# Performance work log

Measured on AMD Instinct MI355X. Metric: run time of the kernel, lower is better.

The kernel has to match this reference:

```python
import jax, jax.numpy as jnp
import numpy as np

HEADS = 8
DIM_HEAD = 64
DIM = 512
B, N = 4, 2048
SCALE = DIM_HEAD ** -0.5


def setup_inputs() -> dict:
    key = jax.random.key(0)
    k1, k2, k3, k4, k5, k6 = jax.random.split(key, 6)
    inner = HEADS * DIM_HEAD
    s = DIM ** -0.5
    return {
        "input_feature": jax.random.normal(k1, (B, N, DIM), dtype=jnp.float32),
        "mask": jax.random.randint(k2, (B, N), 0, 2, dtype=jnp.int32),
        "Wq": jax.random.normal(k3, (inner, DIM), dtype=jnp.float32) * s,
        "Wk": jax.random.normal(k4, (inner, DIM), dtype=jnp.float32) * s,
        "Wv": jax.random.normal(k5, (inner, DIM), dtype=jnp.float32) * s,
        "Wout": jax.random.normal(k6, (DIM, inner), dtype=jnp.float32) * s,
    }


def reference(input_feature, mask, Wq, Wk, Wv, Wout):
    # Conv1d with kernel_size=1, no bias == per-token linear: out = W @ x_channels
    q = jnp.einsum('bnc,dc->bnd', input_feature, Wq)  # [B, N, H*Dh]
    k = jnp.einsum('bnc,dc->bnd', input_feature, Wk)
    v = jnp.einsum('bnc,dc->bnd', input_feature, Wv)

    # '(n c)' channel layout is head-major -> reshape to [B, N, H, Dh], move head out front
    def split_heads(t):
        return t.reshape(B, N, HEADS, DIM_HEAD).transpose(2, 0, 1, 3)  # [H, B, N, Dh]

    q, k, v = split_heads(q), split_heads(k), split_heads(v)

    scores = jnp.einsum('hbtd,hbsd->hbts', q, k) * SCALE  # [H, B, N, N]
    # masked_fill(mask == 0, 1e-9): fill with small CONSTANT (not -inf), faithful to source
    m = (mask == 0)[None, :, None, :]  # [1, B, 1, N]
    scores = jnp.where(m, jnp.float32(1e-9), scores)
    att = jax.nn.softmax(scores, axis=-1)
    out = jnp.einsum('hbts,hbsd->hbtd', att, v)  # [H, B, N, Dh]

    # '(n b) tokens c -> b (n c) tokens' : head-major channel concat
    out = out.transpose(1, 2, 0, 3).reshape(B, N, HEADS * DIM_HEAD)  # [B, N, H*Dh]
    out = jnp.einsum('bnd,ed->bne', out, Wout)  # [B, N, DIM]
    return out
```

## Files before the change

kernel.cpp:

```cpp
#include <hip/hip_runtime.h>
#include <hip/hip_bf16.h>

typedef __attribute__((ext_vector_type(8))) short short8;
typedef __attribute__((ext_vector_type(4))) short short4_t;
typedef __attribute__((ext_vector_type(4))) float float4_;

#define LOG2E 1.4426950408889634f

__device__ __forceinline__ short f2bf(float f) {
    unsigned int u = __builtin_bit_cast(unsigned int, f);
    u = (u + 0x7FFFu + ((u >> 16) & 1u)) >> 16;
    return (short)u;
}

__device__ __forceinline__ unsigned pk2bf(float a, float b) {
    unsigned ua = __builtin_bit_cast(unsigned, a) + 0x8000u;
    unsigned ub = __builtin_bit_cast(unsigned, b) + 0x8000u;
    return __builtin_amdgcn_perm(ub, ua, 0x07060302);
}

__device__ __forceinline__ void pl32swap(unsigned &a, unsigned &b) {
    auto r = __builtin_amdgcn_permlane32_swap(a, b, false, false);
    a = r[0]; b = r[1];
}
__device__ __forceinline__ void pl16swap(unsigned &a, unsigned &b) {
    auto r = __builtin_amdgcn_permlane16_swap(a, b, false, false);
    a = r[0]; b = r[1];
}

union U4 { unsigned u[4]; short8 s; };

__device__ __forceinline__ void gload_lds16(const short* g, short* l) {
    __builtin_amdgcn_global_load_lds((const __attribute__((address_space(1))) void*)g,
                                     (__attribute__((address_space(3))) void*)l, 16, 0, 0);
}

__global__ __launch_bounds__(256) void cvt_kernel(
    const float* __restrict__ X, const float* __restrict__ Wq, const float* __restrict__ Wk,
    const float* __restrict__ Wv, const float* __restrict__ Wo,
    short* __restrict__ Xb, short* __restrict__ Wqkvb, short* __restrict__ Wob) {
    int i = blockIdx.x * 256 + threadIdx.x;
    const float* src; short* dst; float sc = 1.0f;
    if (i < 1048576) { src = X + (size_t)i * 4; dst = Xb + (size_t)i * 4; }
    else {
        int w = i - 1048576; int sec = w >> 16; int j = (w & 65535) * 4;
        if (sec == 0)      { src = Wq + j; dst = Wqkvb + j; sc = 0.125f * LOG2E; }
        else if (sec == 1) { src = Wk + j; dst = Wqkvb + 262144 + j; }
        else if (sec == 2) { src = Wv + j; dst = Wqkvb + 524288 + j; }
        else               { src = Wo + j; dst = Wob + j; }
    }
    float4 v = *(const float4*)src;
    short4_t o;
    o[0] = f2bf(v.x * sc); o[1] = f2bf(v.y * sc); o[2] = f2bf(v.z * sc); o[3] = f2bf(v.w * sc);
    *(short4_t*)dst = o;
}

__global__ __launch_bounds__(256) void gemm_qkv(const short* __restrict__ A, const short* __restrict__ B,
                                                const int* __restrict__ mask,
                                                short* __restrict__ Qb, short* __restrict__ Kb,
                                                short* __restrict__ Vtb) {
    __shared__ __align__(16) short smemAB[2 * 8192];
    __shared__ int maskL[128];
    short* At = smemAB;
    short* Bt = smemAB + 8192;
    constexpr int K = 512;
    int tid = threadIdx.x;
    int wid = tid >> 6, lane = tid & 63;
    int quad = lane >> 4, cc = lane & 15;
    int c7 = cc & 7;
    int wr = wid >> 1, wc = wid & 1;
    int m0 = blockIdx.y * 128, n0 = blockIdx.x * 128;
    if (tid < 128) maskL[tid] = mask[m0 + tid];

    const short* gA[4]; const short* gB[4]; int lofs[4];
#pragma unroll
    for (int p = 0; p < 4; ++p) {
        int slot = p * 256 + tid;
        int r = slot >> 3, c = slot & 7;
        int cs = (c ^ (r & 7)) * 8;
        gA[p] = A + (size_t)(m0 + r) * K + cs;
        gB[p] = B + (size_t)(n0 + r) * K + cs;
        lofs[p] = slot * 8;
    }
    short8 arg[4], brg[4];
#pragma unroll
    for (int p = 0; p < 4; ++p) { arg[p] = *(const short8*)gA[p]; brg[p] = *(const short8*)gB[p]; }

    float4_ acc[4][4] = {};

    for (int kk = 0; kk < K; kk += 64) {
        __syncthreads();
#pragma unroll
        for (int p = 0; p < 4; ++p) {
            *(short8*)(At + lofs[p]) = arg[p];
            *(short8*)(Bt + lofs[p]) = brg[p];
        }
        if (kk < K - 64) {
#pragma unroll
            for (int p = 0; p < 4; ++p) {
                arg[p] = *(const short8*)(gA[p] + kk + 64);
                brg[p] = *(const short8*)(gB[p] + kk + 64);
            }
        }
        __syncthreads();
#pragma unroll
        for (int kc = 0; kc < 2; ++kc) {
            short8 af[4], bf[4];
#pragma unroll
            for (int i = 0; i < 4; ++i)
                af[i] = *(const short8*)(At + (wr * 64 + i * 16 + cc) * 64 + (((kc * 4 + quad) ^ c7) * 8));
#pragma unroll
            for (int j = 0; j < 4; ++j)
                bf[j] = *(const short8*)(Bt + (wc * 64 + j * 16 + cc) * 64 + (((kc * 4 + quad) ^ c7) * 8));
#pragma unroll
            for (int i = 0; i < 4; ++i)
#pragma unroll
                for (int j = 0; j < 4; ++j)
                    acc[i][j] = __builtin_amdgcn_mfma_f32_16x16x32_bf16(af[i], bf[j], acc[i][j], 0, 0, 0);
        }
    }

    int which = n0 >> 9;
    int b = m0 >> 11;
    if (which == 2) {
        __syncthreads();
        short* T = smemAB;
#pragma unroll
        for (int i = 0; i < 4; ++i) {
#pragma unroll
            for (int j = 0; j < 4; ++j) {
                int d_l = wc * 64 + j * 16 + cc;
                int nnb = wr * 64 + i * 16 + quad * 4;
                int G = nnb >> 3, half = (nnb >> 2) & 1;
                int Gs = G ^ (d_l & 15);
                short4_t pv;
                pv[0] = f2bf(acc[i][j][0]); pv[1] = f2bf(acc[i][j][1]);
                pv[2] = f2bf(acc[i][j][2]); pv[3] = f2bf(acc[i][j][3]);
                *(short4_t*)(T + d_l * 128 + Gs * 8 + half * 4) = pv;
            }
        }
        __syncthreads();
#pragma unroll
        for (int p = 0; p < 8; ++p) {
            int slot = p * 256 + tid;
            int d = slot >> 4, G = slot & 15;
            short8 v = *(const short8*)(T + d * 128 + ((G ^ (d & 15)) * 8));
            *(short8*)(Vtb + ((size_t)(b * 512 + (n0 & 511) + d)) * 2048 + (m0 & 2047) + G * 8) = v;
        }
    } else {
        short* dst = which ? Kb : Qb;
#pragma unroll
        for (int i = 0; i < 4; ++i) {
#pragma unroll
            for (int j = 0; j < 4; ++j) {
#pragma unroll
                for (int r = 0; r < 4; ++r) {
                    int lm = wr * 64 + i * 16 + quad * 4 + r;
                    int nn = (m0 & 2047) + lm;
                    int hd = (n0 & 511) + wc * 64 + j * 16 + cc;
                    int h = hd >> 6, dh = hd & 63;
                    float v = acc[i][j][r];
                    if (which == 1 && maskL[lm] == 0) v = 0.0f;
                    dst[((((size_t)b * 8 + h) * 2048 + nn) * 64) + dh] = f2bf(v);
                }
            }
        }
    }
}

__global__ __launch_bounds__(256, 4) void attn_kernel(const short* __restrict__ Q, const short* __restrict__ Kg,
                                                      const short* __restrict__ Vt,
                                                      short* __restrict__ AO) {
    __shared__ __align__(16) short KbufL[2 * 4096];
    __shared__ __align__(16) short VbufL[2 * 4096];

    int tid = threadIdx.x;
    int w = tid >> 6, lane = tid & 63;
    int quad = lane >> 4, cc = lane & 15;
    int c7 = cc & 7;
    int bh = blockIdx.x, b = bh >> 3, h = bh & 7;
    int t0 = blockIdx.y * 64 + w * 16;
    size_t kbase = (size_t)bh * 2048 * 64;
    size_t vbase = (size_t)b * 512 * 2048 + (size_t)h * 64 * 2048;

    short8 qf[2];
#pragma unroll
    for (int kc = 0; kc < 2; ++kc)
        qf[kc] = *(const short8*)(Q + kbase + (size_t)(t0 + cc) * 64 + kc * 32 + quad * 8);

    int koff[4][2];
#pragma unroll
    for (int rb = 0; rb < 4; ++rb)
#pragma unroll
        for (int kc = 0; kc < 2; ++kc)
            koff[rb][kc] = (rb * 16 + cc) * 64 + (((kc * 4 + quad) ^ c7) * 8);

    int sA = tid >> 3, cA = tid & 7;
    const short* gK0 = Kg + kbase + (size_t)sA * 64 + ((cA ^ (sA & 7)) * 8);
    const short* gK1 = gK0 + 32 * 64;
    const short* gV0 = Vt + vbase + (size_t)sA * 2048 + ((cA ^ (sA & 7)) * 8);
    const short* gV1 = gV0 + 32 * 2048;
    int ld0 = tid * 8, ld1 = tid * 8 + 2048;

    short8 krg0 = *(const short8*)gK0, krg1 = *(const short8*)gK1;
    short8 vrg0 = *(const short8*)gV0, vrg1 = *(const short8*)gV1;
    gK0 += 4096; gK1 += 4096; gV0 += 64; gV1 += 64;
    *(short8*)(KbufL + ld0) = krg0; *(short8*)(KbufL + ld1) = krg1;
    *(short8*)(VbufL + ld0) = vrg0; *(short8*)(VbufL + ld1) = vrg1;
    krg0 = *(const short8*)gK0; krg1 = *(const short8*)gK1;
    vrg0 = *(const short8*)gV0; vrg1 = *(const short8*)gV1;
    gK0 += 4096; gK1 += 4096; gV0 += 64; gV1 += 64;

    float4_ o[4] = {};
    float lp = 0.f;

#pragma unroll 2
    for (int it = 0; it < 32; ++it) {
        __syncthreads();
        int cur = it & 1;
        const short* Kt  = KbufL + cur * 4096;
        const short* Vtt = VbufL + cur * 4096;
        if (it < 31) {
            short* Kn = KbufL + (cur ^ 1) * 4096;
            short* Vn = VbufL + (cur ^ 1) * 4096;
            *(short8*)(Kn + ld0) = krg0; *(short8*)(Kn + ld1) = krg1;
            *(short8*)(Vn + ld0) = vrg0; *(short8*)(Vn + ld1) = vrg1;
        }
        if (it < 30) {
            krg0 = *(const short8*)gK0; krg1 = *(const short8*)gK1;
            vrg0 = *(const short8*)gV0; vrg1 = *(const short8*)gV1;
            gK0 += 4096; gK1 += 4096; gV0 += 64; gV1 += 64;
        }

        float4_ acc[4];
        __builtin_amdgcn_s_setprio(1);
#pragma unroll
        for (int sb = 0; sb < 4; ++sb) {
            short8 kf0 = *(const short8*)(Kt + koff[sb][0]);
            short8 kf1 = *(const short8*)(Kt + koff[sb][1]);
            float4_ z = {0.f, 0.f, 0.f, 0.f};
            z = __builtin_amdgcn_mfma_f32_16x16x32_bf16(kf0, qf[0], z, 0, 0, 0);
            acc[sb] = __builtin_amdgcn_mfma_f32_16x16x32_bf16(kf1, qf[1], z, 0, 0, 0);
        }
        __builtin_amdgcn_s_setprio(0);

        unsigned Wp[4][2];
#pragma unroll
        for (int sb = 0; sb < 4; ++sb) {
            float x0 = __builtin_amdgcn_exp2f(acc[sb][0]);
            float x1 = __builtin_amdgcn_exp2f(acc[sb][1]);
            float x2 = __builtin_amdgcn_exp2f(acc[sb][2]);
            float x3 = __builtin_amdgcn_exp2f(acc[sb][3]);
            lp += (x0 + x1) + (x2 + x3);
            Wp[sb][0] = pk2bf(x0, x1);
            Wp[sb][1] = pk2bf(x2, x3);
        }

        short8 pa[2];
#pragma unroll
        for (int kc = 0; kc < 2; ++kc) {
            unsigned a0 = Wp[2 * kc][0], a1 = Wp[2 * kc][1];
            unsigned b0 = Wp[2 * kc + 1][0], b1 = Wp[2 * kc + 1][1];
            pl32swap(a0, b0); pl32swap(a1, b1);
            pl16swap(a0, b0); pl16swap(a1, b1);
            U4 u; u.u[0] = a0; u.u[1] = a1; u.u[2] = b0; u.u[3] = b1;
            pa[kc] = u.s;
        }

        __builtin_amdgcn_s_setprio(1);
#pragma unroll
        for (int db = 0; db < 4; ++db) {
            short8 vf0 = *(const short8*)(Vtt + koff[db][0]);
            short8 vf1 = *(const short8*)(Vtt + koff[db][1]);
            o[db] = __builtin_amdgcn_mfma_f32_16x16x32_bf16(pa[0], vf0, o[db], 0, 0, 0);
            o[db] = __builtin_amdgcn_mfma_f32_16x16x32_bf16(pa[1], vf1, o[db], 0, 0, 0);
        }
        __builtin_amdgcn_s_setprio(0);
    }

    float s = lp;
    s += __shfl_xor(s, 16, 64);
    s += __shfl_xor(s, 32, 64);
    float inv = 1.0f / s;
#pragma unroll
    for (int r = 0; r < 4; ++r) {
        int tl = quad * 4 + r;
        float iv = __shfl(inv, tl, 64);
        size_t rowbase = ((size_t)(b * 2048 + t0 + tl)) * 512 + h * 64;
#pragma unroll
        for (int db = 0; db < 4; ++db)
            AO[rowbase + db * 16 + cc] = f2bf(o[db][r] * iv);
    }
}

__global__ __launch_bounds__(256) void gemm_out(const short* __restrict__ A, const short* __restrict__ B,
                                                float* __restrict__ C) {
    __shared__ __align__(16) short smemAB[8192 + 4096];
    short* At = smemAB;
    short* Bt = smemAB + 8192;
    constexpr int K = 512;
    int tid = threadIdx.x;
    int wid = tid >> 6, lane = tid & 63;
    int quad = lane >> 4, cc = lane & 15;
    int c7 = cc & 7;
    int wr = wid >> 1, wc = wid & 1;
    int m0 = blockIdx.y * 128, n0 = blockIdx.x * 64;

    const short* gA[4]; const short* gB[2]; int lofsA[4], lofsB[2];
#pragma unroll
    for (int p = 0; p < 4; ++p) {
        int slot = p * 256 + tid;
        int r = slot >> 3, c = slot & 7;
        int cs = (c ^ (r & 7)) * 8;
        gA[p] = A + (size_t)(m0 + r) * K + cs;
        lofsA[p] = slot * 8;
    }
#pragma unroll
    for (int p = 0; p < 2; ++p) {
        int slot = p * 256 + tid;
        int r = slot >> 3, c = slot & 7;
        int cs = (c ^ (r & 7)) * 8;
        gB[p] = B + (size_t)(n0 + r) * K + cs;
        lofsB[p] = slot * 8;
    }
    short8 arg[4], brg[2];
#pragma unroll
    for (int p = 0; p < 4; ++p) arg[p] = *(const short8*)gA[p];
#pragma unroll
    for (int p = 0; p < 2; ++p) brg[p] = *(const short8*)gB[p];

    float4_ acc[4][2] = {};

    for (int kk = 0; kk < K; kk += 64) {
        __syncthreads();
#pragma unroll
        for (int p = 0; p < 4; ++p) *(short8*)(At + lofsA[p]) = arg[p];
#pragma unroll
        for (int p = 0; p < 2; ++p) *(short8*)(Bt + lofsB[p]) = brg[p];
        if (kk < K - 64) {
#pragma unroll
            for (int p = 0; p < 4; ++p) arg[p] = *(const short8*)(gA[p] + kk + 64);
#pragma unroll
            for (int p = 0; p < 2; ++p) brg[p] = *(const short8*)(gB[p] + kk + 64);
        }
        __syncthreads();
#pragma unroll
        for (int kc = 0; kc < 2; ++kc) {
            short8 af[4], bf[2];
#pragma unroll
            for (int i = 0; i < 4; ++i)
                af[i] = *(const short8*)(At + (wr * 64 + i * 16 + cc) * 64 + (((kc * 4 + quad) ^ c7) * 8));
#pragma unroll
            for (int j = 0; j < 2; ++j)
                bf[j] = *(const short8*)(Bt + (wc * 32 + j * 16 + cc) * 64 + (((kc * 4 + quad) ^ c7) * 8));
#pragma unroll
            for (int i = 0; i < 4; ++i)
#pragma unroll
                for (int j = 0; j < 2; ++j)
                    acc[i][j] = __builtin_amdgcn_mfma_f32_16x16x32_bf16(af[i], bf[j], acc[i][j], 0, 0, 0);
        }
    }

#pragma unroll
    for (int i = 0; i < 4; ++i)
#pragma unroll
        for (int j = 0; j < 2; ++j)
#pragma unroll
            for (int r = 0; r < 4; ++r) {
                int gm = m0 + wr * 64 + i * 16 + quad * 4 + r;
                int gn = n0 + wc * 32 + j * 16 + cc;
                C[(size_t)gm * 512 + gn] = acc[i][j][r];
            }
}

extern "C" void kernel_launch(void* const* d_in, const int* in_sizes, int n_in,
                              void* d_out, int out_size, void* d_ws, size_t ws_size,
                              hipStream_t stream) {
    const float* X  = (const float*)d_in[0];
    const int* mask = (const int*)d_in[1];
    const float* Wq = (const float*)d_in[2];
    const float* Wk = (const float*)d_in[3];
    const float* Wv = (const float*)d_in[4];
    const float* Wo = (const float*)d_in[5];

    char* ws = (char*)d_ws;
    short* Xbf   = (short*)(ws + 0);
    short* Wqkvb = (short*)(ws + 8388608);
    short* Wob   = (short*)(ws + 9961472);
    short* Qb    = (short*)(ws + 10485760);
    short* Kb    = (short*)(ws + 18874368);
    short* Vtb   = (short*)(ws + 27262976);
    short* AOb   = (short*)(ws + 35651584);

    cvt_kernel<<<5120, 256, 0, stream>>>(X, Wq, Wk, Wv, Wo, Xbf, Wqkvb, Wob);
    gemm_qkv<<<dim3(12, 64), 256, 0, stream>>>(Xbf, Wqkvb, mask, Qb, Kb, Vtb);
    attn_kernel<<<dim3(32, 32), 256, 0, stream>>>(Qb, Kb, Vtb, AOb);
    gemm_out<<<dim3(8, 64), 256, 0, stream>>>(AOb, Wob, (float*)d_out);
}
```

Baseline: 164.5 us.

## Split attention KV tile across wave pairs, each wave handling 32 query rows

Restructures the attention block's work split. Each wave now covers 32 query rows (two 16-row tiles) and half of each 64-key tile, instead of 16 rows over the full key tile. K and V fragments loaded from LDS are reused across two MFMAs, which cuts LDS read traffic per MFMA. The two partial output accumulators and row sums are combined through shared memory at the end. This costs more registers (doubled o accumulators), an extra reduction pass with two barriers, and possibly lower occupancy.

```diff
diff --git a/kernel.cpp b/kernel.cpp
--- a/kernel.cpp
+++ b/kernel.cpp
@@ -171,29 +171,38 @@
 __global__ __launch_bounds__(256, 4) void attn_kernel(const short* __restrict__ Q, const short* __restrict__ Kg,
                                                       const short* __restrict__ Vt,
                                                       short* __restrict__ AO) {
-    __shared__ __align__(16) short KbufL[2 * 4096];
-    __shared__ __align__(16) short VbufL[2 * 4096];
+    __shared__ __align__(16) char smem[32768];
+    short* KbufL = (short*)smem;
+    short* VbufL = (short*)(smem + 16384);
 
     int tid = threadIdx.x;
     int w = tid >> 6, lane = tid & 63;
     int quad = lane >> 4, cc = lane & 15;
     int c7 = cc & 7;
+    int th = w & 1, sh = w >> 1;
     int bh = blockIdx.x, b = bh >> 3, h = bh & 7;
-    int t0 = blockIdx.y * 64 + w * 16;
+    int t0 = blockIdx.y * 64;
+    int tw0 = t0 + th * 32;
     size_t kbase = (size_t)bh * 2048 * 64;
     size_t vbase = (size_t)b * 512 * 2048 + (size_t)h * 64 * 2048;
 
-    short8 qf[2];
-#pragma unroll
-    for (int kc = 0; kc < 2; ++kc)
-        qf[kc] = *(const short8*)(Q + kbase + (size_t)(t0 + cc) * 64 + kc * 32 + quad * 8);
-
-    int koff[4][2];
-#pragma unroll
-    for (int rb = 0; rb < 4; ++rb)
+    short8 qf[2][2];
+#pragma unroll
+    for (int tb = 0; tb < 2; ++tb)
 #pragma unroll
         for (int kc = 0; kc < 2; ++kc)
-            koff[rb][kc] = (rb * 16 + cc) * 64 + (((kc * 4 + quad) ^ c7) * 8);
+            qf[tb][kc] = *(const short8*)(Q + kbase + (size_t)(tw0 + tb * 16 + cc) * 64 + kc * 32 + quad * 8);
+
+    int koff[2][2];
+#pragma unroll
+    for (int sb = 0; sb < 2; ++sb)
+#pragma unroll
+        for (int kc = 0; kc < 2; ++kc)
+            koff[sb][kc] = ((sh * 2 + sb) * 16 + cc) * 64 + (((kc * 4 + quad) ^ c7) * 8);
+    int voff[4];
+#pragma unroll
+    for (int db = 0; db < 4; ++db)
+        voff[db] = (db * 16 + cc) * 64 + (((sh * 4 + quad) ^ c7) * 8);
 
     int sA = tid >> 3, cA = tid & 7;
     const short* gK0 = Kg + kbase + (size_t)sA * 64 + ((cA ^ (sA & 7)) * 8);
@@ -211,8 +220,8 @@
     vrg0 = *(const short8*)gV0; vrg1 = *(const short8*)gV1;
     gK0 += 4096; gK1 += 4096; gV0 += 64; gV1 += 64;
 
-    float4_ o[4] = {};
-    float lp = 0.f;
+    float4_ o[2][4] = {};
+    float lp[2] = {0.f, 0.f};
 
 #pragma unroll 2
     for (int it = 0; it < 32; ++it) {
@@ -232,65 +241,104 @@
             gK0 += 4096; gK1 += 4096; gV0 += 64; gV1 += 64;
         }
 
-        float4_ acc[4];
+        float4_ acc[2][2];
         __builtin_amdgcn_s_setprio(1);
 #pragma unroll
-        for (int sb = 0; sb < 4; ++sb) {
+        for (int sb = 0; sb < 2; ++sb) {
             short8 kf0 = *(const short8*)(Kt + koff[sb][0]);
             short8 kf1 = *(const short8*)(Kt + koff[sb][1]);
-            float4_ z = {0.f, 0.f, 0.f, 0.f};
-            z = __builtin_amdgcn_mfma_f32_16x16x32_bf16(kf0, qf[0], z, 0, 0, 0);
-            acc[sb] = __builtin_amdgcn_mfma_f32_16x16x32_bf16(kf1, qf[1], z, 0, 0, 0);
+#pragma unroll
+            for (int tb = 0; tb < 2; ++tb) {
+                float4_ z = {0.f, 0.f, 0.f, 0.f};
+                z = __builtin_amdgcn_mfma_f32_16x16x32_bf16(kf0, qf[tb][0], z, 0, 0, 0);
+                acc[sb][tb] = __builtin_amdgcn_mfma_f32_16x16x32_bf16(kf1, qf[tb][1], z, 0, 0, 0);
+            }
         }
         __builtin_amdgcn_s_setprio(0);
 
-        unsigned Wp[4][2];
-#pragma unroll
-        for (int sb = 0; sb < 4; ++sb) {
-            float x0 = __builtin_amdgcn_exp2f(acc[sb][0]);
-            float x1 = __builtin_amdgcn_exp2f(acc[sb][1]);
-            float x2 = __builtin_amdgcn_exp2f(acc[sb][2]);
-            float x3 = __builtin_amdgcn_exp2f(acc[sb][3]);
-            lp += (x0 + x1) + (x2 + x3);
-            Wp[sb][0] = pk2bf(x0, x1);
-            Wp[sb][1] = pk2bf(x2, x3);
-        }
+        unsigned Wp[2][2][2];
+#pragma unroll
+        for (int sb = 0; sb < 2; ++sb)
+#pragma unroll
+            for (int tb = 0; tb < 2; ++tb) {
+                float x0 = __builtin_amdgcn_exp2f(acc[sb][tb][0]);
+                float x1 = __builtin_amdgcn_exp2f(acc[sb][tb][1]);
+                float x2 = __builtin_amdgcn_exp2f(acc[sb][tb][2]);
+                float x3 = __builtin_amdgcn_exp2f(acc[sb][tb][3]);
+                lp[tb] += (x0 + x1) + (x2 + x3);
+                Wp[sb][tb][0] = pk2bf(x0, x1);
+                Wp[sb][tb][1] = pk2bf(x2, x3);
+            }
 
         short8 pa[2];
 #pragma unroll
-        for (int kc = 0; kc < 2; ++kc) {
-            unsigned a0 = Wp[2 * kc][0], a1 = Wp[2 * kc][1];
-            unsigned b0 = Wp[2 * kc + 1][0], b1 = Wp[2 * kc + 1][1];
+        for (int tb = 0; tb < 2; ++tb) {
+            unsigned a0 = Wp[0][tb][0], a1 = Wp[0][tb][1];
+            unsigned b0 = Wp[1][tb][0], b1 = Wp[1][tb][1];
             pl32swap(a0, b0); pl32swap(a1, b1);
             pl16swap(a0, b0); pl16swap(a1, b1);
             U4 u; u.u[0] = a0; u.u[1] = a1; u.u[2] = b0; u.u[3] = b1;
-            pa[kc] = u.s;
+            pa[tb] = u.s;
         }
 
         __builtin_amdgcn_s_setprio(1);
 #pragma unroll
         for (int db = 0; db < 4; ++db) {
-            short8 vf0 = *(const short8*)(Vtt + koff[db][0]);
-            short8 vf1 = *(const short8*)(Vtt + koff[db][1]);
-            o[db] = __builtin_amdgcn_mfma_f32_16x16x32_bf16(pa[0], vf0, o[db], 0, 0, 0);
-            o[db] = __builtin_amdgcn_mfma_f32_16x16x32_bf16(pa[1], vf1, o[db], 0, 0, 0);
+            short8 vf = *(const short8*)(Vtt + voff[db]);
+#pragma unroll
+            for (int tb = 0; tb < 2; ++tb)
+                o[tb][db] = __builtin_amdgcn_mfma_f32_16x16x32_bf16(pa[tb], vf, o[tb][db], 0, 0, 0);
         }
         __builtin_amdgcn_s_setprio(0);
     }
 
-    float s = lp;
-    s += __shfl_xor(s, 16, 64);
-    s += __shfl_xor(s, 32, 64);
-    float inv = 1.0f / s;
-#pragma unroll
-    for (int r = 0; r < 4; ++r) {
-        int tl = quad * 4 + r;
-        float iv = __shfl(inv, tl, 64);
-        size_t rowbase = ((size_t)(b * 2048 + t0 + tl)) * 512 + h * 64;
-#pragma unroll
-        for (int db = 0; db < 4; ++db)
-            AO[rowbase + db * 16 + cc] = f2bf(o[db][r] * iv);
-    }
+#pragma unroll
+    for (int tb = 0; tb < 2; ++tb) {
+        lp[tb] += __shfl_xor(lp[tb], 16, 64);
+        lp[tb] += __shfl_xor(lp[tb], 32, 64);
+    }
+    __syncthreads();
+    float* OL = (float*)smem;
+    float* LL = (float*)(smem + 16384);
+
+#pragma unroll
+    for (int tb = 0; tb < 2; ++tb)
+#pragma unroll
+        for (int j = 0; j < 2; ++j) {
+            int db = (sh ^ 1) * 2 + j;
+            int d = db * 16 + cc;
+#pragma unroll
+            for (int r = 0; r < 4; ++r) {
+                int t = tb * 16 + quad * 4 + r;
+                OL[th * 2048 + t * 64 + d] = o[tb][db][r];
+            }
+        }
+    if (lane < 16) {
+#pragma unroll
+        for (int tb = 0; tb < 2; ++tb) LL[sh * 64 + th * 32 + tb * 16 + lane] = lp[tb];
+    }
+    __syncthreads();
+
+    float inv[2];
+#pragma unroll
+    for (int tb = 0; tb < 2; ++tb)
+        inv[tb] = 1.0f / (lp[tb] + LL[(sh ^ 1) * 64 + th * 32 + tb * 16 + cc]);
+
+#pragma unroll
+    for (int tb = 0; tb < 2; ++tb)
+#pragma unroll
+        for (int r = 0; r < 4; ++r) {
+            int t = tb * 16 + quad * 4 + r;
+            float iv = __shfl(inv[tb], quad * 4 + r, 64);
+            size_t rowbase = ((size_t)(b * 2048 + t0 + th * 32 + t)) * 512 + h * 64;
+#pragma unroll
+            for (int j = 0; j < 2; ++j) {
+                int db = sh * 2 + j;
+                int d = db * 16 + cc;
+                float v = o[tb][db][r] + OL[th * 2048 + t * 64 + d];
+                AO[rowbase + d] = f2bf(v * iv);
+            }
+        }
 }
 
 __global__ __launch_bounds__(256) void gemm_out(const short* __restrict__ A, const short* __restrict__ B,
```

New measurement: 173.1 us. +5.2%, slower.
